# Kernel optimization log

Measured on AMD Instinct MI355X. Metric: run time of the kernel, lower is better.

Reference implementation:

```python
import jax, jax.numpy as jnp
import numpy as np


def _lap_min(a):
    """Jonker-Volgenant style Hungarian on cost matrix a (n x m, n <= m), minimizing.
    Returns (rows, cols) of the optimal assignment (len n)."""
    n, m = a.shape
    INF = 1e18
    u = np.zeros(n + 1)
    v = np.zeros(m + 1)
    p = np.zeros(m + 1, dtype=np.int64)   # p[j] = row matched to column j (1-based), 0 = free
    way = np.zeros(m + 1, dtype=np.int64)
    for i in range(1, n + 1):
        p[0] = i
        j0 = 0
        minv = np.full(m + 1, INF)
        used = np.zeros(m + 1, dtype=bool)
        while True:
            used[j0] = True
            i0 = p[j0]
            cur = a[i0 - 1] - u[i0] - v[1:]
            free = ~used[1:]
            upd = free & (cur < minv[1:])
            minv[1:][upd] = cur[upd]
            way[1:][upd] = j0
            mv = np.where(free, minv[1:], INF)
            j1 = int(np.argmin(mv)) + 1
            delta = mv[j1 - 1]
            idx = np.where(used)[0]
            u[p[idx]] += delta
            v[idx] -= delta
            minv[1:][free] -= delta
            j0 = j1
            if p[j0] == 0:
                break
        while j0:
            j1 = way[j0]
            p[j0] = p[j1]
            j0 = j1
    rows = p[1:] - 1
    cols = np.arange(m)
    sel = rows >= 0
    return rows[sel], cols[sel]


def _hungarian(scores, n1s, n2s):
    """Batched max-score LAP on scores[b, :n1, :n2]; returns binary [B,N,M] assignment."""
    B, N, M = scores.shape
    out = np.zeros((B, N, M), dtype=np.float32)
    for b in range(B):
        n, m = int(n1s[b]), int(n2s[b])
        sub = -scores[b, :n, :m].astype(np.float64)
        if n <= m:
            rows, cols = _lap_min(sub)
        else:
            cols, rows = _lap_min(sub.T)
        out[b, rows, cols] = 1.0
    return out


def _loss(pred, gt, dis, pred_ns, gt_ns):
    ali = dis + gt
    ali = jnp.where(ali > 1.0, jnp.float32(0.9), ali)
    p = ali * pred
    g = ali * gt
    N = pred.shape[1]
    M = pred.shape[2]
    mask = (jnp.arange(N)[None, :, None] < pred_ns[:, None, None]) & \
           (jnp.arange(M)[None, None, :] < gt_ns[:, None, None])
    # torch F.binary_cross_entropy clamps log terms at -100
    bce = -(g * jnp.clip(jnp.log(p), -100.0, None)
            + (1.0 - g) * jnp.clip(jnp.log1p(-p), -100.0, None))
    loss = jnp.sum(jnp.where(mask, bce, 0.0))
    n_sum = jnp.sum(pred_ns).astype(pred.dtype)
    return loss / n_sum


def setup_inputs() -> dict:
    B, N = 2048, 64
    key = jax.random.key(0)
    k1, _ = jax.random.split(key)
    # soft doubly-stochastic-ish prediction, strictly inside (0,1)
    pred = 0.01 + 0.98 * jax.random.uniform(k1, (B, N, N), dtype=jnp.float32)
    rng = np.random.default_rng(0)
    ns = rng.integers(N // 2, N + 1, size=B).astype(np.int32)
    gt = np.zeros((B, N, N), dtype=np.float32)
    for b in range(B):
        n = int(ns[b])
        perm = rng.permutation(n)
        gt[b, np.arange(n), perm] = 1.0
    return {"pred_perm": pred, "gt_perm": jnp.asarray(gt),
            "pred_ns": jnp.asarray(ns), "gt_ns": jnp.asarray(ns)}


def reference(pred_perm, gt_perm, pred_ns, gt_ns):
    # Hungarian is discrete (non-differentiable) and runs on host, as in the original
    dis = jnp.asarray(_hungarian(np.asarray(pred_perm),
                                 np.asarray(pred_ns), np.asarray(gt_ns)))
    return _loss(pred_perm, gt_perm, dis, pred_ns, gt_ns)
```

## Files before the change

kernel.cpp:

```cpp
#include <hip/hip_runtime.h>
#include <hip/hip_bf16.h>

#define NMAX 64

typedef float f32x32 __attribute__((ext_vector_type(32)));

__device__ __forceinline__ double readlane_d(double x, int l) {
    const int lo = __builtin_amdgcn_readlane(__double2loint(x), l);
    const int hi = __builtin_amdgcn_readlane(__double2hiint(x), l);
    return __hiloint2double(hi, lo);
}
__device__ __forceinline__ float readlane_f(float x, int l) {
    return __int_as_float(__builtin_amdgcn_readlane(__float_as_int(x), l));
}
template <int CTRL>
__device__ __forceinline__ unsigned dpp_umin(unsigned x) {
    const unsigned t = (unsigned)__builtin_amdgcn_update_dpp(0, (int)x, CTRL, 0xF, 0xF, true);
    return x < t ? x : t;
}
__device__ __forceinline__ unsigned dpp_umin6(unsigned x) {
    x = dpp_umin<0xB1>(x);  x = dpp_umin<0x4E>(x);
    x = dpp_umin<0x141>(x); x = dpp_umin<0x140>(x);
    x = dpp_umin<0x142>(x); x = dpp_umin<0x143>(x);
    return x;
}
template <int CTRL>
__device__ __forceinline__ double dpp_add_step(double x) {
    const int lo = __builtin_amdgcn_update_dpp(0, __double2loint(x), CTRL, 0xF, 0xF, true);
    const int hi = __builtin_amdgcn_update_dpp(0, __double2hiint(x), CTRL, 0xF, 0xF, true);
    return x + __hiloint2double(hi, lo);
}
__device__ __forceinline__ double wave_sum_f64(double x) {
    x = dpp_add_step<0xB1>(x);  x = dpp_add_step<0x4E>(x);
    x = dpp_add_step<0x141>(x); x = dpp_add_step<0x140>(x);
    x = dpp_add_step<0x142>(x); x = dpp_add_step<0x143>(x);
    return readlane_d(x, 63);
}
__device__ __forceinline__ unsigned sel_u32(unsigned long long m, unsigned a, unsigned b) {
    unsigned r;
    asm("v_cndmask_b32 %0, %1, %2, %3" : "=v"(r) : "v"(b), "v"(a), "s"(m));
    return r;
}
__device__ __forceinline__ float sel_f32(unsigned long long m, float a, float b) {
    return __int_as_float((int)sel_u32(m, (unsigned)__float_as_int(a),
                                          (unsigned)__float_as_int(b)));
}
__device__ __forceinline__ int sel_i32(unsigned long long m, int a, int b) {
    return (int)sel_u32(m, (unsigned)a, (unsigned)b);
}
__device__ __forceinline__ float mat_get(const f32x32& lo, const f32x32& hi, int rr) {
    const float aL = lo[rr & 31], aH = hi[rr & 31];
    return (rr & 32) ? aH : aL;
}

__global__ __launch_bounds__(64, 2) void hung_loss_kernel(
    const float* __restrict__ pred, const float* __restrict__ gt,
    const int* __restrict__ n1s, const int* __restrict__ n2s,
    double* __restrict__ partial)
{
    const int b = blockIdx.x;
    const int lane = threadIdx.x & 63;
    const float* __restrict__ predb = pred + (size_t)b * NMAX * NMAX;
    const float* __restrict__ gtb   = gt   + (size_t)b * NMAX * NMAX;
    const int n1 = n1s[b];
    const int n2 = n2s[b];
    const bool trans = (n1 > n2);
    const int n = trans ? n2 : n1;
    const int m = trans ? n1 : n2;
    const float FINF  = __int_as_float(0x7f800000);
    const float FNINF = __int_as_float(0xff800000);

    f32x32 alo, ahi;
    if (!trans) {
        #pragma unroll
        for (int r = 0; r < 32; ++r) alo[r] = predb[r * NMAX + lane];
        #pragma unroll
        for (int r = 0; r < 32; ++r) ahi[r] = predb[(r + 32) * NMAX + lane];
    } else {
        #pragma unroll
        for (int r = 0; r < 32; ++r) alo[r] = predb[lane * NMAX + r];
        #pragma unroll
        for (int r = 0; r < 32; ++r) ahi[r] = predb[lane * NMAX + 32 + r];
    }
    if (lane >= m) {
        #pragma unroll
        for (int r = 0; r < 32; ++r) { alo[r] = FNINF; ahi[r] = FNINF; }
    }

    float v;
    int am = 0;
    {
        float mx = FNINF;
        #pragma unroll
        for (int r = 0; r < 32; ++r) {
            const bool take = (r < n) && (alo[r] > mx);
            mx = take ? alo[r] : mx;
            am = take ? r : am;
        }
        #pragma unroll
        for (int r = 0; r < 32; ++r) {
            const bool take = ((r + 32) < n) && (ahi[r] > mx);
            mx = take ? ahi[r] : mx;
            am = take ? (r + 32) : am;
        }
        v = (lane < m) ? (-mx) : 0.0f;
    }

    __shared__ int mincol[NMAX];
    mincol[lane] = 127;
    __syncthreads();
    if (lane < m) atomicMin(&mincol[am], lane);
    __syncthreads();
    const bool matched = (lane < m) && (mincol[am] == lane);
    int p = matched ? (am + 1) : 0;
    const unsigned long long rowsM =
        __ballot((lane < n) && (mincol[lane] != 127));
    unsigned long long freerows =
        (~rowsM) & ((n == 64) ? ~0ull : ((1ull << n) - 1ull));

    float u = 0.0f;
    float uent = 0.0f;
    float dsel = 0.0f;
    const unsigned VMASK = 0xFFFFFFC0u;

    {
        int steps = 0;
        while (freerows && steps < 128) {
            ++steps;
            const int i = __ffsll(freerows);
            freerows &= freerows - 1;
            const float a = mat_get(alo, ahi, i - 1);
            float r_ = (0.0f - a) - v;
            r_ = fmaxf(r_, 0.0f);
            const unsigned key1 = (__float_as_uint(r_) & VMASK) | (unsigned)lane;
            const unsigned K1 = (unsigned)__builtin_amdgcn_readlane((int)dpp_umin6(key1), 63);
            const int j1 = (int)(K1 & 63u) + 1;
            const unsigned key2 = sel_u32(1ull << (j1 - 1), 0xFFFFFFFFu, key1);
            const unsigned K2 = (unsigned)__builtin_amdgcn_readlane((int)dpp_umin6(key2), 63);
            const unsigned u1b = K1 & VMASK, u2b = K2 & VMASK;
            const float u2f = __uint_as_float(u2b);
            int jt = j1;
            int i0k = __builtin_amdgcn_readlane(p, j1 - 1);
            if (u1b < u2b) {
                const float u1f = __uint_as_float(u1b);
                v = sel_f32(1ull << (j1 - 1), v - (u2f - u1f), v);
            } else if (i0k != 0) {
                jt = (int)(K2 & 63u) + 1;
                i0k = __builtin_amdgcn_readlane(p, jt - 1);
            }
            p = sel_i32(1ull << (jt - 1), i, p);
            u = sel_f32(1ull << (i - 1), u2f, u);
            if (i0k != 0) freerows |= 1ull << (i0k - 1);
        }
    }

    while (freerows) {
        const int i = __ffsll(freerows);
        freerows &= freerows - 1;
        unsigned long long um = 0ull;
        unsigned long long rowm = 1ull << (i - 1);
        float d = FINF;
        int way = 0;
        int vj0 = 0;
        float s = 0.0f - readlane_f(u, i - 1);
        uent = sel_f32(rowm, 0.0f, uent);
        float aval = mat_get(alo, ahi, i - 1);
        int j1f = 0;
        float DT = 0.0f;
        for (int guard = 0; guard < NMAX; ++guard) {
            const float r_ = (0.0f - aval) - v;
            const float cur = fmaxf(r_ + s, 0.0f);
            const float dn = fminf(d, cur);
            const unsigned key = (__float_as_uint(dn) & VMASK) | (unsigned)lane;
            const unsigned K = (unsigned)__builtin_amdgcn_readlane((int)dpp_umin6(key), 63);
            const int j1 = (int)(K & 63u) + 1;
            const int i0n = __builtin_amdgcn_readlane(p, j1 - 1);
            const float H = __uint_as_float(K & VMASK);
            const unsigned long long mj = 1ull << (j1 - 1);
            const bool lt = cur < d;
            way  = lt ? vj0 : way;
            dsel = sel_f32(mj, dn, dsel);
            d    = sel_f32(mj, FINF, dn);
            if (i0n == 0) { j1f = j1; DT = H; break; }
            um |= mj;
            rowm |= 1ull << (i0n - 1);
            uent = sel_f32(1ull << (i0n - 1), H, uent);
            s = H - readlane_f(u, i0n - 1);
            aval = mat_get(alo, ahi, i0n - 1);
            aval = __int_as_float((int)sel_u32(um, 0xFF800000u, __float_as_int(aval)));
            vj0 = j1;
        }
        v = sel_f32(um,   v + (dsel - DT), v);
        u = sel_f32(rowm, u + (DT - uent), u);
        int j0 = j1f;
        while (j0 > 0) {
            const int j1w = __builtin_amdgcn_readlane(way, j0 - 1);
            const int newp = (j1w == 0) ? i : __builtin_amdgcn_readlane(p, j1w - 1);
            p = sel_i32(1ull << (j0 - 1), newp, p);
            j0 = j1w;
        }
    }

    double lsum = 0.0;
    if (!trans) {
        #pragma unroll
        for (int i2 = 0; i2 < NMAX; ++i2) {
            const float pv = (i2 < 32) ? alo[i2] : ahi[i2 - 32];
            const float gv = gtb[i2 * NMAX + lane];
            const float dis = (p == i2 + 1) ? 1.0f : 0.0f;
            float ali = dis + gv;
            if (ali > 1.0f) ali = 0.9f;
            const float pp = ali * pv;
            const float gg = ali * gv;
            const float lp  = fmaxf(logf(pp),    -100.0f);
            const float l1p = fmaxf(log1pf(-pp), -100.0f);
            const float bce = -(gg * lp + (1.0f - gg) * l1p);
            if (i2 < n1 && lane < n2) lsum += (double)bce;
        }
    } else {
        for (int i2 = 0; i2 < NMAX; ++i2) {
            const float pv = predb[i2 * NMAX + lane];
            const float gv = gtb[i2 * NMAX + lane];
            const int pi = __builtin_amdgcn_readlane(p, i2);
            const float dis = (pi - 1 == lane) ? 1.0f : 0.0f;
            float ali = dis + gv;
            if (ali > 1.0f) ali = 0.9f;
            const float pp = ali * pv;
            const float gg = ali * gv;
            const float lp  = fmaxf(logf(pp),    -100.0f);
            const float l1p = fmaxf(log1pf(-pp), -100.0f);
            const float bce = -(gg * lp + (1.0f - gg) * l1p);
            if (i2 < n1 && lane < n2) lsum += (double)bce;
        }
    }
    const double tsum = wave_sum_f64(lsum);
    if (lane == 0) partial[b] = tsum;
}

__global__ __launch_bounds__(256) void finalize_kernel(
    const double* __restrict__ partial, const int* __restrict__ n1s,
    float* __restrict__ out, int B)
{
    __shared__ double sred[256];
    __shared__ int    nred[256];
    const int t = threadIdx.x;
    double s = 0.0;
    int ns = 0;
    for (int bb = t; bb < B; bb += 256) { s += partial[bb]; ns += n1s[bb]; }
    sred[t] = s; nred[t] = ns;
    __syncthreads();
    for (int off = 128; off >= 1; off >>= 1) {
        if (t < off) { sred[t] += sred[t + off]; nred[t] += nred[t + off]; }
        __syncthreads();
    }
    if (t == 0) out[0] = (float)sred[0] / (float)nred[0];
}

extern "C" void kernel_launch(void* const* d_in, const int* in_sizes, int n_in,
                              void* d_out, int out_size, void* d_ws, size_t ws_size,
                              hipStream_t stream) {
    const float* pred = (const float*)d_in[0];
    const float* gt   = (const float*)d_in[1];
    const int* n1s    = (const int*)d_in[2];
    const int* n2s    = (const int*)d_in[3];
    float* out = (float*)d_out;
    double* partial = (double*)d_ws;
    const int B = in_sizes[2];

    hung_loss_kernel<<<B, 64, 0, stream>>>(pred, gt, n1s, n2s, partial);
    finalize_kernel<<<1, 256, 0, stream>>>(partial, n1s, out, B);
}
```

Baseline: 111.2 us.

## Stage cost matrix in padded LDS instead of per-lane register vectors

Replaces the two 32-wide register vectors holding each lane's matrix column with a padded shared-memory tile loaded via coalesced float4 reads, transposed on store when needed. Row lookups in the Hungarian loops become LDS reads, and columns beyond m are masked with a precomputed bitmask instead of being overwritten with -inf. The aim is to avoid dynamic indexing into register vectors, which likely compiled to long select chains or scratch spills, and to cut register pressure. In exchange every inner-loop row fetch now pays LDS latency, and the prologue adds a barrier.

Result: slower. 127.5 us (+14.6%).

```diff
diff --git a/kernel.cpp b/kernel.cpp
--- a/kernel.cpp
+++ b/kernel.cpp
@@ -2,8 +2,7 @@
 #include <hip/hip_bf16.h>
 
 #define NMAX 64
-
-typedef float f32x32 __attribute__((ext_vector_type(32)));
+#define LDA 65
 
 __device__ __forceinline__ double readlane_d(double x, int l) {
     const int lo = __builtin_amdgcn_readlane(__double2loint(x), l);
@@ -47,10 +46,6 @@
 }
 __device__ __forceinline__ int sel_i32(unsigned long long m, int a, int b) {
     return (int)sel_u32(m, (unsigned)a, (unsigned)b);
-}
-__device__ __forceinline__ float mat_get(const f32x32& lo, const f32x32& hi, int rr) {
-    const float aL = lo[rr & 31], aH = hi[rr & 31];
-    return (rr & 32) ? aH : aL;
 }
 
 __global__ __launch_bounds__(64, 2) void hung_loss_kernel(
@@ -69,46 +64,42 @@
     const int m = trans ? n1 : n2;
     const float FINF  = __int_as_float(0x7f800000);
     const float FNINF = __int_as_float(0xff800000);
-
-    f32x32 alo, ahi;
-    if (!trans) {
+    const unsigned NEGINF32 = 0xFF800000u;
+
+    __shared__ float A[NMAX * LDA];
+    __shared__ int mincol[NMAX];
+    mincol[lane] = 127;
+    {
+        const float4* p4 = (const float4*)predb;
         #pragma unroll
-        for (int r = 0; r < 32; ++r) alo[r] = predb[r * NMAX + lane];
-        #pragma unroll
-        for (int r = 0; r < 32; ++r) ahi[r] = predb[(r + 32) * NMAX + lane];
-    } else {
-        #pragma unroll
-        for (int r = 0; r < 32; ++r) alo[r] = predb[lane * NMAX + r];
-        #pragma unroll
-        for (int r = 0; r < 32; ++r) ahi[r] = predb[lane * NMAX + 32 + r];
-    }
-    if (lane >= m) {
-        #pragma unroll
-        for (int r = 0; r < 32; ++r) { alo[r] = FNINF; ahi[r] = FNINF; }
-    }
+        for (int it = 0; it < 16; ++it) {
+            const float4 val = p4[it * 64 + lane];
+            const int r = it * 4 + (lane >> 4);
+            const int c = (lane & 15) * 4;
+            if (!trans) {
+                A[r * LDA + c + 0] = val.x; A[r * LDA + c + 1] = val.y;
+                A[r * LDA + c + 2] = val.z; A[r * LDA + c + 3] = val.w;
+            } else {
+                A[(c + 0) * LDA + r] = val.x; A[(c + 1) * LDA + r] = val.y;
+                A[(c + 2) * LDA + r] = val.z; A[(c + 3) * LDA + r] = val.w;
+            }
+        }
+    }
+    __syncthreads();
 
     float v;
     int am = 0;
     {
         float mx = FNINF;
-        #pragma unroll
-        for (int r = 0; r < 32; ++r) {
-            const bool take = (r < n) && (alo[r] > mx);
-            mx = take ? alo[r] : mx;
+        for (int r = 0; r < n; ++r) {
+            const float a = A[r * LDA + lane];
+            const bool take = a > mx;
+            mx = take ? a : mx;
             am = take ? r : am;
         }
-        #pragma unroll
-        for (int r = 0; r < 32; ++r) {
-            const bool take = ((r + 32) < n) && (ahi[r] > mx);
-            mx = take ? ahi[r] : mx;
-            am = take ? (r + 32) : am;
-        }
         v = (lane < m) ? (-mx) : 0.0f;
     }
 
-    __shared__ int mincol[NMAX];
-    mincol[lane] = 127;
-    __syncthreads();
     if (lane < m) atomicMin(&mincol[am], lane);
     __syncthreads();
     const bool matched = (lane < m) && (mincol[am] == lane);
@@ -121,6 +112,7 @@
     float u = 0.0f;
     float uent = 0.0f;
     float dsel = 0.0f;
+    const unsigned long long fake = (m < 64) ? (~0ull << m) : 0ull;
     const unsigned VMASK = 0xFFFFFFC0u;
 
     {
@@ -129,7 +121,8 @@
             ++steps;
             const int i = __ffsll(freerows);
             freerows &= freerows - 1;
-            const float a = mat_get(alo, ahi, i - 1);
+            float a = A[(i - 1) * LDA + lane];
+            a = __int_as_float((int)sel_u32(fake, NEGINF32, __float_as_int(a)));
             float r_ = (0.0f - a) - v;
             r_ = fmaxf(r_, 0.0f);
             const unsigned key1 = (__float_as_uint(r_) & VMASK) | (unsigned)lane;
@@ -157,14 +150,15 @@
     while (freerows) {
         const int i = __ffsll(freerows);
         freerows &= freerows - 1;
-        unsigned long long um = 0ull;
+        unsigned long long um = fake;
         unsigned long long rowm = 1ull << (i - 1);
         float d = FINF;
         int way = 0;
         int vj0 = 0;
         float s = 0.0f - readlane_f(u, i - 1);
         uent = sel_f32(rowm, 0.0f, uent);
-        float aval = mat_get(alo, ahi, i - 1);
+        float aval = A[(i - 1) * LDA + lane];
+        aval = __int_as_float((int)sel_u32(um, NEGINF32, __float_as_int(aval)));
         int j1f = 0;
         float DT = 0.0f;
         for (int guard = 0; guard < NMAX; ++guard) {
@@ -186,8 +180,8 @@
             rowm |= 1ull << (i0n - 1);
             uent = sel_f32(1ull << (i0n - 1), H, uent);
             s = H - readlane_f(u, i0n - 1);
-            aval = mat_get(alo, ahi, i0n - 1);
-            aval = __int_as_float((int)sel_u32(um, 0xFF800000u, __float_as_int(aval)));
+            aval = A[(i0n - 1) * LDA + lane];
+            aval = __int_as_float((int)sel_u32(um, NEGINF32, __float_as_int(aval)));
             vj0 = j1;
         }
         v = sel_f32(um,   v + (dsel - DT), v);
@@ -203,9 +197,8 @@
 
     double lsum = 0.0;
     if (!trans) {
-        #pragma unroll
         for (int i2 = 0; i2 < NMAX; ++i2) {
-            const float pv = (i2 < 32) ? alo[i2] : ahi[i2 - 32];
+            const float pv = A[i2 * LDA + lane];
             const float gv = gtb[i2 * NMAX + lane];
             const float dis = (p == i2 + 1) ? 1.0f : 0.0f;
             float ali = dis + gv;
```

## Precompute per-row top-two reduced costs and reuse them in auction augmentation

Applied to the files above, without the earlier changes.

Stages the cost matrix in shared memory (padded stride, transposed when needed) so each lane can scan its own row and precompute the smallest and second-smallest reduced cost. The augmenting-row-reduction loop then reads these cached minima by readlane and only recomputes them with two wave-wide DPP min reductions when a column price involved has changed since the cache was built. The step cap rises from 128 to 192. In exchange the kernel pays a 64-iteration serial scan per lane, a 16.6 KB shared allocation that may reduce occupancy, and extra bookkeeping. Cached values use full float precision rather than the masked keys, so tie decisions can differ slightly from before.

Measured after the change: 149.0 us. +34.0%, slower.

```diff
diff --git a/kernel.cpp b/kernel.cpp
--- a/kernel.cpp
+++ b/kernel.cpp
@@ -2,6 +2,7 @@
 #include <hip/hip_bf16.h>
 
 #define NMAX 64
+#define LDA 65
 
 typedef float f32x32 __attribute__((ext_vector_type(32)));
 
@@ -69,6 +70,27 @@
     const int m = trans ? n1 : n2;
     const float FINF  = __int_as_float(0x7f800000);
     const float FNINF = __int_as_float(0xff800000);
+    const unsigned NEGINF32 = 0xFF800000u;
+
+    __shared__ float A[NMAX * LDA];
+    __shared__ int mincol[NMAX];
+    mincol[lane] = 127;
+    {
+        const float4* p4 = (const float4*)predb;
+        #pragma unroll
+        for (int it = 0; it < 16; ++it) {
+            const float4 val = p4[it * 64 + lane];
+            const int r = it * 4 + (lane >> 4);
+            const int c = (lane & 15) * 4;
+            if (!trans) {
+                A[r * LDA + c + 0] = val.x; A[r * LDA + c + 1] = val.y;
+                A[r * LDA + c + 2] = val.z; A[r * LDA + c + 3] = val.w;
+            } else {
+                A[(c + 0) * LDA + r] = val.x; A[(c + 1) * LDA + r] = val.y;
+                A[(c + 2) * LDA + r] = val.z; A[(c + 3) * LDA + r] = val.w;
+            }
+        }
+    }
 
     f32x32 alo, ahi;
     if (!trans) {
@@ -106,8 +128,6 @@
         v = (lane < m) ? (-mx) : 0.0f;
     }
 
-    __shared__ int mincol[NMAX];
-    mincol[lane] = 127;
     __syncthreads();
     if (lane < m) atomicMin(&mincol[am], lane);
     __syncthreads();
@@ -121,36 +141,66 @@
     float u = 0.0f;
     float uent = 0.0f;
     float dsel = 0.0f;
+    const unsigned long long fake = (m < 64) ? (~0ull << m) : 0ull;
     const unsigned VMASK = 0xFFFFFFC0u;
 
+    float bm1 = FINF, bm2 = FINF;
+    int bj1 = 1, bj2 = 1;
+    #pragma unroll
+    for (int c = 0; c < NMAX; ++c) {
+        const float vc = readlane_f(v, c);
+        const float a  = A[lane * LDA + c];
+        float rc = fmaxf((0.0f - a) - vc, 0.0f);
+        if ((fake >> c) & 1ull) rc = FINF;
+        const bool b1 = rc < bm1;
+        const bool b2 = rc < bm2;
+        bm2 = b1 ? bm1 : (b2 ? rc : bm2);
+        bj2 = b1 ? bj1 : (b2 ? (c + 1) : bj2);
+        bm1 = b1 ? rc : bm1;
+        bj1 = b1 ? (c + 1) : bj1;
+    }
+
     {
+        unsigned long long vchanged = 0ull;
         int steps = 0;
-        while (freerows && steps < 128) {
+        while (freerows && steps < 192) {
             ++steps;
             const int i = __ffsll(freerows);
             freerows &= freerows - 1;
-            const float a = mat_get(alo, ahi, i - 1);
-            float r_ = (0.0f - a) - v;
-            r_ = fmaxf(r_, 0.0f);
-            const unsigned key1 = (__float_as_uint(r_) & VMASK) | (unsigned)lane;
-            const unsigned K1 = (unsigned)__builtin_amdgcn_readlane((int)dpp_umin6(key1), 63);
-            const int j1 = (int)(K1 & 63u) + 1;
-            const unsigned key2 = sel_u32(1ull << (j1 - 1), 0xFFFFFFFFu, key1);
-            const unsigned K2 = (unsigned)__builtin_amdgcn_readlane((int)dpp_umin6(key2), 63);
-            const unsigned u1b = K1 & VMASK, u2b = K2 & VMASK;
-            const float u2f = __uint_as_float(u2b);
+            int j1 = __builtin_amdgcn_readlane(bj1, i - 1);
+            int j2 = __builtin_amdgcn_readlane(bj2, i - 1);
+            float u1 = readlane_f(bm1, i - 1);
+            float u2 = readlane_f(bm2, i - 1);
+            bool tie = !(u1 < u2);
+            const bool bad = ((vchanged >> (j1 - 1)) & 1ull) ||
+                             (tie && ((vchanged >> (j2 - 1)) & 1ull));
+            if (bad) {
+                const float aa = mat_get(alo, ahi, i - 1);
+                const float r_ = fmaxf((0.0f - aa) - v, 0.0f);
+                const unsigned key = (__float_as_uint(r_) & VMASK) | (unsigned)lane;
+                const unsigned K1 =
+                    (unsigned)__builtin_amdgcn_readlane((int)dpp_umin6(key), 63);
+                j1 = (int)(K1 & 63u) + 1;
+                const unsigned key2s = sel_u32(1ull << (j1 - 1), 0xFFFFFFFFu, key);
+                const unsigned K2 =
+                    (unsigned)__builtin_amdgcn_readlane((int)dpp_umin6(key2s), 63);
+                j2 = (int)(K2 & 63u) + 1;
+                u1 = __uint_as_float(K1 & VMASK);
+                u2 = __uint_as_float(K2 & VMASK);
+                tie = !(u1 < u2);
+            }
             int jt = j1;
-            int i0k = __builtin_amdgcn_readlane(p, j1 - 1);
-            if (u1b < u2b) {
-                const float u1f = __uint_as_float(u1b);
-                v = sel_f32(1ull << (j1 - 1), v - (u2f - u1f), v);
-            } else if (i0k != 0) {
-                jt = (int)(K2 & 63u) + 1;
-                i0k = __builtin_amdgcn_readlane(p, jt - 1);
+            int kick = __builtin_amdgcn_readlane(p, j1 - 1);
+            if (!tie) {
+                v = sel_f32(1ull << (j1 - 1), v - (u2 - u1), v);
+                vchanged |= 1ull << (j1 - 1);
+            } else if (kick != 0) {
+                jt = j2;
+                kick = __builtin_amdgcn_readlane(p, j2 - 1);
             }
             p = sel_i32(1ull << (jt - 1), i, p);
-            u = sel_f32(1ull << (i - 1), u2f, u);
-            if (i0k != 0) freerows |= 1ull << (i0k - 1);
+            u = sel_f32(1ull << (i - 1), u2, u);
+            if (kick != 0) freerows |= 1ull << (kick - 1);
         }
     }
 
@@ -187,7 +237,7 @@
             uent = sel_f32(1ull << (i0n - 1), H, uent);
             s = H - readlane_f(u, i0n - 1);
             aval = mat_get(alo, ahi, i0n - 1);
-            aval = __int_as_float((int)sel_u32(um, 0xFF800000u, __float_as_int(aval)));
+            aval = __int_as_float((int)sel_u32(um, NEGINF32, __float_as_int(aval)));
             vj0 = j1;
         }
         v = sel_f32(um,   v + (dsel - DT), v);
```
